# Performance work log

Hardware: AMD Instinct MI355X
Metric: run time of the kernel (lower is better)

## Reference

```python
import jax, jax.numpy as jnp
import numpy as np

D = 2048
H = 16
KV = 4
DH = D // H  # 128
REP = H // KV
ROPE_BASE = 10000.0


def _rope(x, pos):
    # x: (B, h, L, Dh), pos: (L,)
    half = x.shape[-1] // 2
    inv_freq = 1.0 / (ROPE_BASE ** (jnp.arange(0, half, dtype=jnp.float32) / half))
    ang = pos.astype(jnp.float32)[:, None] * inv_freq[None, :]          # (L, half)
    cos = jnp.concatenate([jnp.cos(ang), jnp.cos(ang)], axis=-1)        # (L, Dh)
    sin = jnp.concatenate([jnp.sin(ang), jnp.sin(ang)], axis=-1)
    x1, x2 = x[..., :half], x[..., half:]
    rot = jnp.concatenate([-x2, x1], axis=-1)
    return x * cos[None, None] + rot * sin[None, None]


def setup_inputs() -> dict:
    key = jax.random.key(0)
    ks = jax.random.split(key, 5)
    s = 1.0 / np.sqrt(D)
    return {
        "x": jax.random.normal(ks[0], (2, 2048, D), dtype=jnp.float32),
        "wq": jax.random.uniform(ks[1], (H * DH, D), jnp.float32, -s, s),
        "wk": jax.random.uniform(ks[2], (KV * DH, D), jnp.float32, -s, s),
        "wv": jax.random.uniform(ks[3], (KV * DH, D), jnp.float32, -s, s),
        "wo": jax.random.uniform(ks[4], (D, H * DH), jnp.float32, -s, s),
    }


def reference(x, wq, wk, wv, wo):
    B, T, _ = x.shape
    q = (x @ wq.T).reshape(B, T, H, DH).transpose(0, 2, 1, 3)    # (B,H,T,Dh)
    k = (x @ wk.T).reshape(B, T, KV, DH).transpose(0, 2, 1, 3)   # (B,KV,T,Dh)
    v = (x @ wv.T).reshape(B, T, KV, DH).transpose(0, 2, 1, 3)
    Tc = T  # no kv cache
    pos = jnp.arange(Tc)
    q = _rope(q, pos)
    k = _rope(k, pos)
    # GQA: repeat kv heads to match query heads
    k_full = jnp.repeat(k, REP, axis=1)                          # (B,H,Tc,Dh)
    v_full = jnp.repeat(v, REP, axis=1)
    scale = 1.0 / np.sqrt(DH)
    scores = jnp.einsum('bhtd,bhsd->bhts', q, k_full) * scale    # (B,H,T,Tc)
    row = jnp.arange(T)[:, None]
    col = jnp.arange(Tc)[None, :]
    causal = col <= row + (Tc - T)
    scores = jnp.where(causal[None, None], scores, -jnp.inf)
    attn = jax.nn.softmax(scores, axis=-1)
    out = jnp.einsum('bhts,bhsd->bhtd', attn, v_full)            # (B,H,T,Dh)
    out = out.transpose(0, 2, 1, 3).reshape(B, T, H * DH)
    return out @ wo.T
```

## Files before the change

kernel.cpp:

```cpp
#include <hip/hip_runtime.h>

typedef float f32x4 __attribute__((ext_vector_type(4)));
typedef short s16x8 __attribute__((ext_vector_type(8)));
typedef unsigned short u16;

__device__ __forceinline__ u16 f2bf(float f) {
    union { float f; unsigned u; } v; v.f = f;
    return (u16)((v.u + 0x7fffu + ((v.u >> 16) & 1u)) >> 16);
}
__device__ __forceinline__ float bf2f(u16 h) {
    union { unsigned u; float f; } v; v.u = ((unsigned)h) << 16;
    return v.f;
}
__device__ __forceinline__ float fast_exp2(float x) {
#if __has_builtin(__builtin_amdgcn_exp2f)
    return __builtin_amdgcn_exp2f(x);
#else
    return exp2f(x);
#endif
}

__device__ __forceinline__ void gload_lds16(const void* g, void* l) {
    __builtin_amdgcn_global_load_lds((__attribute__((address_space(1))) void*)g,
                                     (__attribute__((address_space(3))) void*)l, 16, 0, 0);
}

__global__ __launch_bounds__(256) void cvt_all(const float* __restrict__ x,  const float* __restrict__ wq,
                                               const float* __restrict__ wk, const float* __restrict__ wv,
                                               u16* __restrict__ xb, u16* __restrict__ wqkvb) {
    int u = blockIdx.x * 256 + threadIdx.x;
    const float* src;
    u16* dst;
    if (u < 1048576) { src = x + (size_t)u * 8; dst = xb + (size_t)u * 8; }
    else {
        int w = u - 1048576;
        dst = wqkvb + (size_t)w * 8;
        if (w < 524288)      src = wq + (size_t)w * 8;
        else if (w < 655360) src = wk + (size_t)(w - 524288) * 8;
        else                 src = wv + (size_t)(w - 655360) * 8;
    }
    const float4* p = (const float4*)src;
    float4 a = p[0], b = p[1];
    s16x8 o;
    o[0] = f2bf(a.x); o[1] = f2bf(a.y); o[2] = f2bf(a.z); o[3] = f2bf(a.w);
    o[4] = f2bf(b.x); o[5] = f2bf(b.y); o[6] = f2bf(b.z); o[7] = f2bf(b.w);
    *(s16x8*)dst = o;
}

__global__ __launch_bounds__(256) void cvt_kernel(const float* __restrict__ in,
                                                  u16* __restrict__ out, int n8) {
    int i = blockIdx.x * 256 + threadIdx.x;
    if (i >= n8) return;
    const float4* p = (const float4*)(in + (size_t)i * 8);
    float4 a = p[0], b = p[1];
    s16x8 o;
    o[0] = f2bf(a.x); o[1] = f2bf(a.y); o[2] = f2bf(a.z); o[3] = f2bf(a.w);
    o[4] = f2bf(b.x); o[5] = f2bf(b.y); o[6] = f2bf(b.z); o[7] = f2bf(b.w);
    *(s16x8*)(out + (size_t)i * 8) = o;
}

__global__ __launch_bounds__(256) void norm_comb(const float* __restrict__ Oacc,
                                                 const float* __restrict__ Lacc,
                                                 u16* __restrict__ ab) {
    int i = blockIdx.x * 256 + threadIdx.x;
    int g = i >> 15;
    int rem = i & 32767;
    int qti = rem >> 10;
    int rem2 = rem & 1023;
    int row = rem2 >> 6;
    int colblk = rem2 & 63;
    int col0 = colblk * 8;
    int head = colblk >> 4;
    size_t tile0 = (size_t)(g * 32 + qti);
    size_t tile1 = (size_t)((8 + g) * 32 + qti);
    const float* p0 = Oacc + tile0 * 8192 + row * 512 + col0;
    const float* p1 = Oacc + tile1 * 8192 + row * 512 + col0;
    float L0 = Lacc[(tile0 * 4 + head) * 16 + row];
    float L1 = Lacc[(tile1 * 4 + head) * 16 + row];
    float inv = 1.0f / (L0 + L1);
    int b = g >> 2, kv = g & 3;
    int token = (96 + qti) * 16 + row;
    u16* pd = ab + ((size_t)(b * 2048 + token) << 11) + kv * 512 + col0;
    float4 a0 = ((const float4*)p0)[0], a1 = ((const float4*)p0)[1];
    float4 b0 = ((const float4*)p1)[0], b1 = ((const float4*)p1)[1];
    s16x8 o;
    o[0] = f2bf((a0.x + b0.x) * inv); o[1] = f2bf((a0.y + b0.y) * inv);
    o[2] = f2bf((a0.z + b0.z) * inv); o[3] = f2bf((a0.w + b0.w) * inv);
    o[4] = f2bf((a1.x + b1.x) * inv); o[5] = f2bf((a1.y + b1.y) * inv);
    o[6] = f2bf((a1.z + b1.z) * inv); o[7] = f2bf((a1.w + b1.w) * inv);
    *(s16x8*)pd = o;
}

template<int OUT>
__global__ __launch_bounds__(256) void gemm128(const u16* __restrict__ A, const u16* __restrict__ B,
                                               void* __restrict__ C, void* __restrict__ Ck,
                                               void* __restrict__ Cv, int M, int N, int K) {
    __shared__ __align__(16) u16 Ald[128 * 64];
    __shared__ __align__(16) u16 Bld[128 * 64];
    const int t = threadIdx.x, wid = t >> 6, lane = t & 63;
    const int m0 = blockIdx.y * 128, n0 = blockIdx.x * 128;
    const int ml = lane & 15, quad = lane >> 4, m7 = ml & 7;
    const int wm = (wid & 1) * 64, wn = (wid >> 1) * 64;
    const int sr = lane >> 3, sc = lane & 7;

    f32x4 acc[4][4] = {};

    for (int k0 = 0; k0 < K; k0 += 64) {
        if (k0) __syncthreads();
        #pragma unroll
        for (int i = 0; i < 4; ++i) {
            int seg = wid * 4 + i;
            int r = seg * 8 + sr;
            int c = (sc ^ (r & 7)) * 8;
            gload_lds16(A + (size_t)(m0 + r) * K + k0 + c, &Ald[seg * 512]);
            gload_lds16(B + (size_t)(n0 + r) * K + k0 + c, &Bld[seg * 512]);
        }
        __syncthreads();
        #pragma unroll
        for (int kk = 0; kk < 64; kk += 32) {
            s16x8 af[4], bf[4];
            #pragma unroll
            for (int mi = 0; mi < 4; ++mi)
                af[mi] = *(const s16x8*)&Ald[(wm + mi * 16 + ml) * 64 + (((kk >> 3) + quad) ^ m7) * 8];
            #pragma unroll
            for (int ni = 0; ni < 4; ++ni)
                bf[ni] = *(const s16x8*)&Bld[(wn + ni * 16 + ml) * 64 + (((kk >> 3) + quad) ^ m7) * 8];
            #pragma unroll
            for (int mi = 0; mi < 4; ++mi)
                #pragma unroll
                for (int ni = 0; ni < 4; ++ni)
                    acc[mi][ni] = __builtin_amdgcn_mfma_f32_16x16x32_bf16(af[mi], bf[ni], acc[mi][ni], 0, 0, 0);
        }
    }
    #pragma unroll
    for (int mi = 0; mi < 4; ++mi)
        #pragma unroll
        for (int ni = 0; ni < 4; ++ni) {
            int gmb = m0 + wm + mi * 16 + quad * 4;
            int gn  = n0 + wn + ni * 16 + ml;
            if constexpr (OUT == 4) {
                if (n0 < 2048) {
                    #pragma unroll
                    for (int r = 0; r < 4; ++r)
                        ((u16*)C)[(size_t)(gmb + r) * 2048 + gn] = f2bf(acc[mi][ni][r]);
                } else if (n0 < 2560) {
                    #pragma unroll
                    for (int r = 0; r < 4; ++r)
                        ((u16*)Ck)[(size_t)(gmb + r) * 512 + (gn - 2048)] = f2bf(acc[mi][ni][r]);
                } else {
                    ushort4 v;
                    v.x = f2bf(acc[mi][ni][0]); v.y = f2bf(acc[mi][ni][1]);
                    v.z = f2bf(acc[mi][ni][2]); v.w = f2bf(acc[mi][ni][3]);
                    *(ushort4*)((u16*)Cv + (size_t)(gn - 2560) * M + gmb) = v;
                }
            } else {
                #pragma unroll
                for (int r = 0; r < 4; ++r)
                    ((float*)C)[(size_t)(gmb + r) * N + gn] = acc[mi][ni][r];
            }
        }
}

__global__ __launch_bounds__(256) void rope_kernel(u16* __restrict__ qb, u16* __restrict__ kb,
                                                   int nq, int ntot, float sq) {
    int idx = blockIdx.x * 256 + threadIdx.x;
    if (idx >= ntot) return;
    u16* base; int nheads; float scl; int id;
    if (idx < nq) { base = qb; nheads = 16; scl = sq;  id = idx; }
    else          { base = kb; nheads = 4;  scl = 1.f; id = idx - nq; }
    int i = id & 63;
    int rest = id >> 6;
    int hh = rest % nheads;
    int tok = rest / nheads;
    int tpos = tok & 2047;
    u16* row = base + (size_t)tok * nheads * 128 + hh * 128;
    float x1 = bf2f(row[i]);
    float x2 = bf2f(row[i + 64]);
    float inv = expf(-(float)i * 0.14391156731570787f);
    float ang = (float)tpos * inv;
    float s, c;
    sincosf(ang, &s, &c);
    row[i]      = f2bf((x1 * c - x2 * s) * scl);
    row[i + 64] = f2bf((x2 * c + x1 * s) * scl);
}

__global__ __launch_bounds__(256, 4) void attn_kernel(const u16* __restrict__ Q, const u16* __restrict__ Kb,
                                                      const u16* __restrict__ Vt, u16* __restrict__ O) {
    __shared__ __align__(16) u16 Klds[64 * 128];
    __shared__ __align__(16) u16 Vlds[128 * 64];
    __shared__ __align__(16) u16 Plds[4][16 * 64];
    const int t = threadIdx.x, wslot = t >> 6, lane = t & 63;
    const int kv = blockIdx.y, b = blockIdx.z;
    const int g = kv + 4 * b;
    const int bx = blockIdx.x;
    int qt;
    switch ((g >> 1) & 3) {
        case 0:  qt = bx; break;
        case 1:  qt = 127 - bx; break;
        case 2:  qt = (bx + 64) & 127; break;
        default: qt = (63 - bx) & 127; break;
    }
    const int h = kv * 4 + wslot;
    const int ml = lane & 15, quad = lane >> 4, m7 = ml & 7;
    const int t0 = qt * 16;
    const int n = (qt >> 2) + 1;

    s16x8 qf[4];
    {
        const u16* qp = Q + ((size_t)(b * 2048 + t0 + ml) * 2048 + h * 128);
        #pragma unroll
        for (int kc = 0; kc < 4; ++kc)
            qf[kc] = *(const s16x8*)(qp + kc * 32 + quad * 8);
    }

    s16x8 ones;
    #pragma unroll
    for (int j = 0; j < 8; ++j) ones[j] = (short)0x3F80;

    f32x4 Oa[8] = {};
    f32x4 L = {};

    for (int it = 0; it < n; ++it) {
        const int s0 = it * 64;
        if (it) __syncthreads();
        #pragma unroll
        for (int i = 0; i < 4; ++i) {
            int seg = wslot * 4 + i;
            int kr = seg * 4 + (lane >> 4);
            int kc = ((lane & 15) ^ (kr & 7)) * 8;
            gload_lds16(Kb + (size_t)(b * 2048 + s0 + kr) * 512 + kv * 128 + kc, &Klds[seg * 512]);
            int vr = seg * 8 + (lane >> 3);
            int vc = ((lane & 7) ^ (vr & 7)) * 8;
            gload_lds16(Vt + (size_t)(kv * 128 + vr) * 4096 + b * 2048 + s0 + vc, &Vlds[seg * 512]);
        }
        __syncthreads();

        f32x4 S[4] = {};
        #pragma unroll
        for (int kc = 0; kc < 4; ++kc)
            #pragma unroll
            for (int ti = 0; ti < 4; ++ti) {
                s16x8 kf = *(const s16x8*)&Klds[(ti * 16 + ml) * 128 + ((kc * 4 + quad) ^ m7) * 8];
                S[ti] = __builtin_amdgcn_mfma_f32_16x16x32_bf16(qf[kc], kf, S[ti], 0, 0, 0);
            }

        {
            u16* pl = &Plds[wslot][0];
            const bool diag = (it == n - 1);
            #pragma unroll
            for (int r = 0; r < 4; ++r) {
                int qr = t0 + quad * 4 + r;
                int row = quad * 4 + r;
                #pragma unroll
                for (int ti = 0; ti < 4; ++ti) {
                    float e = fast_exp2(S[ti][r]);
                    if (diag && (s0 + ti * 16 + ml > qr)) e = 0.f;
                    union { float f; unsigned u; } cv; cv.f = e;
                    pl[row * 64 + (((ti * 2 + (ml >> 3)) ^ (row & 7)) * 8) + (ml & 7)] = (u16)(cv.u >> 16);
                }
            }
        }
        asm volatile("s_waitcnt lgkmcnt(0)" ::: "memory");
        s16x8 pf[2];
        pf[0] = *(const s16x8*)&Plds[wslot][ml * 64 + ((quad)     ^ m7) * 8];
        pf[1] = *(const s16x8*)&Plds[wslot][ml * 64 + ((4 + quad) ^ m7) * 8];
        asm volatile("s_waitcnt lgkmcnt(0)" ::: "memory");

        #pragma unroll
        for (int c = 0; c < 2; ++c) {
            #pragma unroll
            for (int nt = 0; nt < 8; ++nt) {
                s16x8 vf = *(const s16x8*)&Vlds[(nt * 16 + ml) * 64 + ((c * 4 + quad) ^ m7) * 8];
                Oa[nt] = __builtin_amdgcn_mfma_f32_16x16x32_bf16(pf[c], vf, Oa[nt], 0, 0, 0);
            }
            L = __builtin_amdgcn_mfma_f32_16x16x32_bf16(pf[c], ones, L, 0, 0, 0);
        }
    }

    #pragma unroll
    for (int nt = 0; nt < 8; ++nt)
        #pragma unroll
        for (int r = 0; r < 4; ++r) {
            int col = h * 128 + nt * 16 + ml;
            O[(size_t)(b * 2048 + t0 + quad * 4 + r) * 2048 + col] = f2bf(Oa[nt][r] / L[r]);
        }
}

__global__ __launch_bounds__(256, 4) void attn_sched(const u16* __restrict__ Q, const u16* __restrict__ Kb,
                                                     const u16* __restrict__ Vt, u16* __restrict__ O,
                                                     float* __restrict__ Oacc, float* __restrict__ Lacc) {
    __shared__ __align__(16) u16 Klds[64 * 128];
    __shared__ __align__(16) u16 Vlds[128 * 64];
    __shared__ __align__(16) u16 Plds[4][16 * 64];
    const int t = threadIdx.x, wslot = t >> 6, lane = t & 63;
    const int bid = blockIdx.x;
    const int idx = bid >> 3, g = bid & 7;
    const int kv = g & 3, b = g >> 2;

    int qt, it0, it1, nfull, hsel = 0;
    bool partial;
    if (idx < 32) {
        qt = 95 - idx; nfull = (qt >> 2) + 1; it0 = 0; it1 = nfull; partial = false;
    } else if (idx < 96) {
        int p = (idx - 32) >> 1; hsel = (idx - 32) & 1;
        qt = 127 - p; nfull = (qt >> 2) + 1;
        int nh = nfull >> 1;
        it0 = hsel ? nh : 0;
        it1 = hsel ? nfull : nh;
        partial = true;
    } else {
        qt = 159 - idx; nfull = (qt >> 2) + 1; it0 = 0; it1 = nfull; partial = false;
    }

    const int h = kv * 4 + wslot;
    const int ml = lane & 15, quad = lane >> 4, m7 = ml & 7;
    const int t0 = qt * 16;

    s16x8 qf[4];
    {
        const u16* qp = Q + ((size_t)(b * 2048 + t0 + ml) * 2048 + h * 128);
        #pragma unroll
        for (int kc = 0; kc < 4; ++kc)
            qf[kc] = *(const s16x8*)(qp + kc * 32 + quad * 8);
    }

    s16x8 ones;
    #pragma unroll
    for (int j = 0; j < 8; ++j) ones[j] = (short)0x3F80;

    f32x4 Oa[8] = {};
    f32x4 L = {};

    for (int it = it0; it < it1; ++it) {
        const int s0 = it * 64;
        if (it != it0) __syncthreads();
        #pragma unroll
        for (int i = 0; i < 4; ++i) {
            int seg = wslot * 4 + i;
            int kr = seg * 4 + (lane >> 4);
            int kc = ((lane & 15) ^ (kr & 7)) * 8;
            gload_lds16(Kb + (size_t)(b * 2048 + s0 + kr) * 512 + kv * 128 + kc, &Klds[seg * 512]);
            int vr = seg * 8 + (lane >> 3);
            int vc = ((lane & 7) ^ (vr & 7)) * 8;
            gload_lds16(Vt + (size_t)(kv * 128 + vr) * 4096 + b * 2048 + s0 + vc, &Vlds[seg * 512]);
        }
        __syncthreads();

        f32x4 S[4] = {};
        #pragma unroll
        for (int kc = 0; kc < 4; ++kc)
            #pragma unroll
            for (int ti = 0; ti < 4; ++ti) {
                s16x8 kf = *(const s16x8*)&Klds[(ti * 16 + ml) * 128 + ((kc * 4 + quad) ^ m7) * 8];
                S[ti] = __builtin_amdgcn_mfma_f32_16x16x32_bf16(qf[kc], kf, S[ti], 0, 0, 0);
            }

        {
            u16* pl = &Plds[wslot][0];
            const bool diag = (it == nfull - 1);
            #pragma unroll
            for (int r = 0; r < 4; ++r) {
                int qr = t0 + quad * 4 + r;
                int row = quad * 4 + r;
                #pragma unroll
                for (int ti = 0; ti < 4; ++ti) {
                    float e = fast_exp2(S[ti][r]);
                    if (diag && (s0 + ti * 16 + ml > qr)) e = 0.f;
                    union { float f; unsigned u; } cv; cv.f = e;
                    pl[row * 64 + (((ti * 2 + (ml >> 3)) ^ (row & 7)) * 8) + (ml & 7)] = (u16)(cv.u >> 16);
                }
            }
        }
        asm volatile("s_waitcnt lgkmcnt(0)" ::: "memory");
        s16x8 pf[2];
        pf[0] = *(const s16x8*)&Plds[wslot][ml * 64 + ((quad)     ^ m7) * 8];
        pf[1] = *(const s16x8*)&Plds[wslot][ml * 64 + ((4 + quad) ^ m7) * 8];
        asm volatile("s_waitcnt lgkmcnt(0)" ::: "memory");

        #pragma unroll
        for (int c = 0; c < 2; ++c) {
            #pragma unroll
            for (int nt = 0; nt < 8; ++nt) {
                s16x8 vf = *(const s16x8*)&Vlds[(nt * 16 + ml) * 64 + ((c * 4 + quad) ^ m7) * 8];
                Oa[nt] = __builtin_amdgcn_mfma_f32_16x16x32_bf16(pf[c], vf, Oa[nt], 0, 0, 0);
            }
            L = __builtin_amdgcn_mfma_f32_16x16x32_bf16(pf[c], ones, L, 0, 0, 0);
        }
    }

    if (!partial) {
        #pragma unroll
        for (int nt = 0; nt < 8; ++nt)
            #pragma unroll
            for (int r = 0; r < 4; ++r) {
                int col = h * 128 + nt * 16 + ml;
                O[(size_t)(b * 2048 + t0 + quad * 4 + r) * 2048 + col] = f2bf(Oa[nt][r] / L[r]);
            }
    } else {
        const int qti = qt - 96;
        float* Ob = Oacc + (size_t)((hsel * 8 + g) * 32 + qti) * 8192;
        #pragma unroll
        for (int nt = 0; nt < 8; ++nt)
            #pragma unroll
            for (int r = 0; r < 4; ++r)
                Ob[(quad * 4 + r) * 512 + wslot * 128 + nt * 16 + ml] = Oa[nt][r];
        if (ml == 0) {
            float* Lb = Lacc + ((size_t)((hsel * 8 + g) * 32 + qti) * 4 + wslot) * 16;
            #pragma unroll
            for (int r = 0; r < 4; ++r)
                Lb[quad * 4 + r] = L[r];
        }
    }
}

extern "C" void kernel_launch(void* const* d_in, const int* in_sizes, int n_in,
                              void* d_out, int out_size, void* d_ws, size_t ws_size,
                              hipStream_t stream) {
    const float* x  = (const float*)d_in[0];
    const float* wq = (const float*)d_in[1];
    const float* wk = (const float*)d_in[2];
    const float* wv = (const float*)d_in[3];
    const float* wo = (const float*)d_in[4];
    float* out = (float*)d_out;
    char* ws = (char*)d_ws;

    const size_t MB = 1024 * 1024;
    u16* xb    = (u16*)(ws);
    u16* qb    = (u16*)(ws + 16 * MB);
    u16* kb    = (u16*)(ws + 32 * MB);
    u16* vtb   = (u16*)(ws + 36 * MB);
    u16* wqkvb = (u16*)(ws + 40 * MB);
    u16* ab    = xb;
    u16* wob   = wqkvb;

    const bool split = ws_size >= 70 * MB;

    cvt_all<<<7168, 256, 0, stream>>>(x, wq, wk, wv, xb, wqkvb);

    gemm128<4><<<dim3(24, 32), 256, 0, stream>>>(xb, wqkvb, qb, kb, vtb, 4096, 3072, 2048);

    cvt_kernel<<<2048, 256, 0, stream>>>(wo, wob, 524288);

    rope_kernel<<<20480, 256, 0, stream>>>(qb, kb, 4194304, 5242880, 0.12751743f);

    if (split) {
        float* Oacc = (float*)(ws + 52 * MB);
        float* Lacc = (float*)(ws + 68 * MB);
        attn_sched<<<1280, 256, 0, stream>>>(qb, kb, vtb, ab, Oacc, Lacc);
        norm_comb<<<1024, 256, 0, stream>>>(Oacc, Lacc, ab);
    } else {
        attn_kernel<<<dim3(128, 4, 2), 256, 0, stream>>>(qb, kb, vtb, ab);
    }

    gemm128<1><<<dim3(16, 32), 256, 0, stream>>>(ab, wob, out, nullptr, nullptr, 4096, 2048, 2048);
}
```

Measured before the change: 323.8 us.

## Process paired 16-row query tiles per block to reuse K/V LDS loads

The attention kernel now handles two 16-row query tiles (32 query rows) per block. Each K/V tile staged in LDS is reused for twice as many MFMA operations, and the grid shrinks from 1280 to 768 blocks with a reworked causal split schedule. Partial accumulators are written into the output buffer as scratch, which lowers the workspace threshold needed to enable the split path. The cost is doubled accumulator registers, with launch bounds lowered to 3 blocks per CU, so occupancy may drop.

```diff
diff --git a/kernel.cpp b/kernel.cpp
--- a/kernel.cpp
+++ b/kernel.cpp
@@ -59,28 +59,27 @@
     *(s16x8*)(out + (size_t)i * 8) = o;
 }
 
-__global__ __launch_bounds__(256) void norm_comb(const float* __restrict__ Oacc,
-                                                 const float* __restrict__ Lacc,
+__global__ __launch_bounds__(256) void norm_comb(const float* __restrict__ Opart,
+                                                 const float* __restrict__ Lpart,
                                                  u16* __restrict__ ab) {
     int i = blockIdx.x * 256 + threadIdx.x;
-    int g = i >> 15;
-    int rem = i & 32767;
-    int qti = rem >> 10;
-    int rem2 = rem & 1023;
-    int row = rem2 >> 6;
-    int colblk = rem2 & 63;
-    int col0 = colblk * 8;
-    int head = colblk >> 4;
-    size_t tile0 = (size_t)(g * 32 + qti);
-    size_t tile1 = (size_t)((8 + g) * 32 + qti);
-    const float* p0 = Oacc + tile0 * 8192 + row * 512 + col0;
-    const float* p1 = Oacc + tile1 * 8192 + row * 512 + col0;
-    float L0 = Lacc[(tile0 * 4 + head) * 16 + row];
-    float L1 = Lacc[(tile1 * 4 + head) * 16 + row];
+    int c0 = (i & 63) * 8;
+    int r2 = i >> 6;
+    int row32 = r2 & 31;
+    int r3 = r2 >> 5;
+    int qsi = r3 & 31;
+    int g = r3 >> 5;
+    int head = c0 >> 7;
+    size_t pi0 = (size_t)(g * 32 + qsi);
+    size_t pi1 = (size_t)((8 + g) * 32 + qsi);
+    const float* p0 = Opart + pi0 * 16384 + row32 * 512 + c0;
+    const float* p1 = Opart + pi1 * 16384 + row32 * 512 + c0;
+    float L0 = Lpart[pi0 * 128 + row32 * 4 + head];
+    float L1 = Lpart[pi1 * 128 + row32 * 4 + head];
     float inv = 1.0f / (L0 + L1);
     int b = g >> 2, kv = g & 3;
-    int token = (96 + qti) * 16 + row;
-    u16* pd = ab + ((size_t)(b * 2048 + token) << 11) + kv * 512 + col0;
+    int token = (32 + qsi) * 32 + row32;
+    u16* pd = ab + ((size_t)(b * 2048 + token) << 11) + kv * 512 + c0;
     float4 a0 = ((const float4*)p0)[0], a1 = ((const float4*)p0)[1];
     float4 b0 = ((const float4*)p1)[0], b1 = ((const float4*)p1)[1];
     s16x8 o;
@@ -286,50 +285,53 @@
         }
 }
 
-__global__ __launch_bounds__(256, 4) void attn_sched(const u16* __restrict__ Q, const u16* __restrict__ Kb,
-                                                     const u16* __restrict__ Vt, u16* __restrict__ O,
-                                                     float* __restrict__ Oacc, float* __restrict__ Lacc) {
+__global__ __launch_bounds__(256, 3) void attn_pair(const u16* __restrict__ Q, const u16* __restrict__ Kb,
+                                                    const u16* __restrict__ Vt, u16* __restrict__ O,
+                                                    float* __restrict__ Opart, float* __restrict__ Lpart) {
     __shared__ __align__(16) u16 Klds[64 * 128];
     __shared__ __align__(16) u16 Vlds[128 * 64];
-    __shared__ __align__(16) u16 Plds[4][16 * 64];
+    __shared__ __align__(16) u16 Plds[4][2][16 * 64];
     const int t = threadIdx.x, wslot = t >> 6, lane = t & 63;
     const int bid = blockIdx.x;
-    const int idx = bid >> 3, g = bid & 7;
+    const int g = bid & 7, idx = bid >> 3;
     const int kv = g & 3, b = g >> 2;
 
-    int qt, it0, it1, nfull, hsel = 0;
+    int qs, it0, it1, n, hsel = 0;
     bool partial;
-    if (idx < 32) {
-        qt = 95 - idx; nfull = (qt >> 2) + 1; it0 = 0; it1 = nfull; partial = false;
-    } else if (idx < 96) {
-        int p = (idx - 32) >> 1; hsel = (idx - 32) & 1;
-        qt = 127 - p; nfull = (qt >> 2) + 1;
-        int nh = nfull >> 1;
+    if (idx < 64) {
+        int p = idx >> 1; hsel = idx & 1;
+        qs = 63 - p; n = (qs >> 1) + 1;
+        int nh = n >> 1;
         it0 = hsel ? nh : 0;
-        it1 = hsel ? nfull : nh;
+        it1 = hsel ? n : nh;
         partial = true;
     } else {
-        qt = 159 - idx; nfull = (qt >> 2) + 1; it0 = 0; it1 = nfull; partial = false;
+        qs = 95 - idx; n = (qs >> 1) + 1;
+        it0 = 0; it1 = n;
+        partial = false;
     }
 
     const int h = kv * 4 + wslot;
     const int ml = lane & 15, quad = lane >> 4, m7 = ml & 7;
-    const int t0 = qt * 16;
-
-    s16x8 qf[4];
+    const int t0a = qs * 32, t0b = qs * 32 + 16;
+
+    s16x8 qfA[4], qfB[4];
     {
-        const u16* qp = Q + ((size_t)(b * 2048 + t0 + ml) * 2048 + h * 128);
-        #pragma unroll
-        for (int kc = 0; kc < 4; ++kc)
-            qf[kc] = *(const s16x8*)(qp + kc * 32 + quad * 8);
+        const u16* qpA = Q + ((size_t)(b * 2048 + t0a + ml) * 2048 + h * 128);
+        const u16* qpB = Q + ((size_t)(b * 2048 + t0b + ml) * 2048 + h * 128);
+        #pragma unroll
+        for (int kc = 0; kc < 4; ++kc) {
+            qfA[kc] = *(const s16x8*)(qpA + kc * 32 + quad * 8);
+            qfB[kc] = *(const s16x8*)(qpB + kc * 32 + quad * 8);
+        }
     }
 
     s16x8 ones;
     #pragma unroll
     for (int j = 0; j < 8; ++j) ones[j] = (short)0x3F80;
 
-    f32x4 Oa[8] = {};
-    f32x4 L = {};
+    f32x4 OA[8] = {}, OB[8] = {};
+    f32x4 LA = {}, LB = {};
 
     for (int it = it0; it < it1; ++it) {
         const int s0 = it * 64;
@@ -346,18 +348,19 @@
         }
         __syncthreads();
 
-        f32x4 S[4] = {};
+        f32x4 Sa[4] = {}, Sb[4] = {};
         #pragma unroll
         for (int kc = 0; kc < 4; ++kc)
             #pragma unroll
             for (int ti = 0; ti < 4; ++ti) {
                 s16x8 kf = *(const s16x8*)&Klds[(ti * 16 + ml) * 128 + ((kc * 4 + quad) ^ m7) * 8];
-                S[ti] = __builtin_amdgcn_mfma_f32_16x16x32_bf16(qf[kc], kf, S[ti], 0, 0, 0);
-            }
-
-        {
-            u16* pl = &Plds[wslot][0];
-            const bool diag = (it == nfull - 1);
+                Sa[ti] = __builtin_amdgcn_mfma_f32_16x16x32_bf16(qfA[kc], kf, Sa[ti], 0, 0, 0);
+                Sb[ti] = __builtin_amdgcn_mfma_f32_16x16x32_bf16(qfB[kc], kf, Sb[ti], 0, 0, 0);
+            }
+
+        const bool diag = (it == n - 1);
+        auto do_soft = [&](f32x4* S, int t0, int pslot) {
+            u16* pl = &Plds[wslot][pslot][0];
             #pragma unroll
             for (int r = 0; r < 4; ++r) {
                 int qr = t0 + quad * 4 + r;
@@ -370,11 +373,15 @@
                     pl[row * 64 + (((ti * 2 + (ml >> 3)) ^ (row & 7)) * 8) + (ml & 7)] = (u16)(cv.u >> 16);
                 }
             }
-        }
+        };
+        do_soft(Sa, t0a, 0);
+        do_soft(Sb, t0b, 1);
         asm volatile("s_waitcnt lgkmcnt(0)" ::: "memory");
-        s16x8 pf[2];
-        pf[0] = *(const s16x8*)&Plds[wslot][ml * 64 + ((quad)     ^ m7) * 8];
-        pf[1] = *(const s16x8*)&Plds[wslot][ml * 64 + ((4 + quad) ^ m7) * 8];
+        s16x8 pfA[2], pfB[2];
+        pfA[0] = *(const s16x8*)&Plds[wslot][0][ml * 64 + ((quad)     ^ m7) * 8];
+        pfA[1] = *(const s16x8*)&Plds[wslot][0][ml * 64 + ((4 + quad) ^ m7) * 8];
+        pfB[0] = *(const s16x8*)&Plds[wslot][1][ml * 64 + ((quad)     ^ m7) * 8];
+        pfB[1] = *(const s16x8*)&Plds[wslot][1][ml * 64 + ((4 + quad) ^ m7) * 8];
         asm volatile("s_waitcnt lgkmcnt(0)" ::: "memory");
 
         #pragma unroll
@@ -382,9 +389,11 @@
             #pragma unroll
             for (int nt = 0; nt < 8; ++nt) {
                 s16x8 vf = *(const s16x8*)&Vlds[(nt * 16 + ml) * 64 + ((c * 4 + quad) ^ m7) * 8];
-                Oa[nt] = __builtin_amdgcn_mfma_f32_16x16x32_bf16(pf[c], vf, Oa[nt], 0, 0, 0);
-            }
-            L = __builtin_amdgcn_mfma_f32_16x16x32_bf16(pf[c], ones, L, 0, 0, 0);
+                OA[nt] = __builtin_amdgcn_mfma_f32_16x16x32_bf16(pfA[c], vf, OA[nt], 0, 0, 0);
+                OB[nt] = __builtin_amdgcn_mfma_f32_16x16x32_bf16(pfB[c], vf, OB[nt], 0, 0, 0);
+            }
+            LA = __builtin_amdgcn_mfma_f32_16x16x32_bf16(pfA[c], ones, LA, 0, 0, 0);
+            LB = __builtin_amdgcn_mfma_f32_16x16x32_bf16(pfB[c], ones, LB, 0, 0, 0);
         }
     }
 
@@ -394,21 +403,27 @@
             #pragma unroll
             for (int r = 0; r < 4; ++r) {
                 int col = h * 128 + nt * 16 + ml;
-                O[(size_t)(b * 2048 + t0 + quad * 4 + r) * 2048 + col] = f2bf(Oa[nt][r] / L[r]);
+                O[(size_t)(b * 2048 + t0a + quad * 4 + r) * 2048 + col] = f2bf(OA[nt][r] / LA[r]);
+                O[(size_t)(b * 2048 + t0b + quad * 4 + r) * 2048 + col] = f2bf(OB[nt][r] / LB[r]);
             }
     } else {
-        const int qti = qt - 96;
-        float* Ob = Oacc + (size_t)((hsel * 8 + g) * 32 + qti) * 8192;
+        const size_t pi = (size_t)((hsel * 8 + g) * 32 + (qs - 32));
+        float* Ob = Opart + pi * 16384;
+        float* Lb = Lpart + pi * 128;
         #pragma unroll
         for (int nt = 0; nt < 8; ++nt)
             #pragma unroll
-            for (int r = 0; r < 4; ++r)
-                Ob[(quad * 4 + r) * 512 + wslot * 128 + nt * 16 + ml] = Oa[nt][r];
+            for (int r = 0; r < 4; ++r) {
+                int c = wslot * 128 + nt * 16 + ml;
+                Ob[(quad * 4 + r) * 512 + c]        = OA[nt][r];
+                Ob[(16 + quad * 4 + r) * 512 + c]   = OB[nt][r];
+            }
         if (ml == 0) {
-            float* Lb = Lacc + ((size_t)((hsel * 8 + g) * 32 + qti) * 4 + wslot) * 16;
-            #pragma unroll
-            for (int r = 0; r < 4; ++r)
-                Lb[quad * 4 + r] = L[r];
+            #pragma unroll
+            for (int r = 0; r < 4; ++r) {
+                Lb[(quad * 4 + r) * 4 + wslot]      = LA[r];
+                Lb[(16 + quad * 4 + r) * 4 + wslot] = LB[r];
+            }
         }
     }
 }
@@ -433,7 +448,7 @@
     u16* ab    = xb;
     u16* wob   = wqkvb;
 
-    const bool split = ws_size >= 70 * MB;
+    const bool split = ws_size >= 53 * MB;
 
     cvt_all<<<7168, 256, 0, stream>>>(x, wq, wk, wv, xb, wqkvb);
 
@@ -444,10 +459,10 @@
     rope_kernel<<<20480, 256, 0, stream>>>(qb, kb, 4194304, 5242880, 0.12751743f);
 
     if (split) {
-        float* Oacc = (float*)(ws + 52 * MB);
-        float* Lacc = (float*)(ws + 68 * MB);
-        attn_sched<<<1280, 256, 0, stream>>>(qb, kb, vtb, ab, Oacc, Lacc);
-        norm_comb<<<1024, 256, 0, stream>>>(Oacc, Lacc, ab);
+        float* Opart = out;
+        float* Lpart = (float*)(ws + 52 * MB);
+        attn_pair<<<768, 256, 0, stream>>>(qb, kb, vtb, ab, Opart, Lpart);
+        norm_comb<<<2048, 256, 0, stream>>>(Opart, Lpart, ab);
     } else {
         attn_kernel<<<dim3(128, 4, 2), 256, 0, stream>>>(qb, kb, vtb, ab);
     }
```

Result: slower. 351.9 us (+8.7%).

## Split attention KV loop for all upper-half query tiles, stage partials in output buffer

Applied to the files above, without the earlier changes.

Extends the split-KV scheme so that all query tiles from 64 to 127 are processed by two half-blocks, where before only tiles 96 to 127 were. Grid size grows from 1280 to 1536 blocks, and norm_comb grows to match. This is meant to balance the causal workload across CUs. The float partial-output buffer now lives in the final output tensor, which the out-projection GEMM later overwrites. That lowers the workspace requirement so the split path is taken more often, at the cost of more partial-sum traffic and more combine work.

```diff
diff --git a/kernel.cpp b/kernel.cpp
--- a/kernel.cpp
+++ b/kernel.cpp
@@ -59,28 +59,27 @@
     *(s16x8*)(out + (size_t)i * 8) = o;
 }
 
-__global__ __launch_bounds__(256) void norm_comb(const float* __restrict__ Oacc,
-                                                 const float* __restrict__ Lacc,
+__global__ __launch_bounds__(256) void norm_comb(const float* __restrict__ Opart,
+                                                 const float* __restrict__ Lpart,
                                                  u16* __restrict__ ab) {
     int i = blockIdx.x * 256 + threadIdx.x;
-    int g = i >> 15;
-    int rem = i & 32767;
-    int qti = rem >> 10;
-    int rem2 = rem & 1023;
-    int row = rem2 >> 6;
-    int colblk = rem2 & 63;
-    int col0 = colblk * 8;
-    int head = colblk >> 4;
-    size_t tile0 = (size_t)(g * 32 + qti);
-    size_t tile1 = (size_t)((8 + g) * 32 + qti);
-    const float* p0 = Oacc + tile0 * 8192 + row * 512 + col0;
-    const float* p1 = Oacc + tile1 * 8192 + row * 512 + col0;
-    float L0 = Lacc[(tile0 * 4 + head) * 16 + row];
-    float L1 = Lacc[(tile1 * 4 + head) * 16 + row];
+    int c0 = (i & 63) * 8;
+    int r = i >> 6;
+    int row = r & 15;
+    int r2 = r >> 4;
+    int qti = r2 & 63;
+    int g = r2 >> 6;
+    int head = c0 >> 7;
+    size_t pi0 = (size_t)(g * 64 + qti);
+    size_t pi1 = (size_t)((8 + g) * 64 + qti);
+    const float* p0 = Opart + pi0 * 8192 + row * 512 + c0;
+    const float* p1 = Opart + pi1 * 8192 + row * 512 + c0;
+    float L0 = Lpart[pi0 * 64 + row * 4 + head];
+    float L1 = Lpart[pi1 * 64 + row * 4 + head];
     float inv = 1.0f / (L0 + L1);
     int b = g >> 2, kv = g & 3;
-    int token = (96 + qti) * 16 + row;
-    u16* pd = ab + ((size_t)(b * 2048 + token) << 11) + kv * 512 + col0;
+    int token = (64 + qti) * 16 + row;
+    u16* pd = ab + ((size_t)(b * 2048 + token) << 11) + kv * 512 + c0;
     float4 a0 = ((const float4*)p0)[0], a1 = ((const float4*)p0)[1];
     float4 b0 = ((const float4*)p1)[0], b1 = ((const float4*)p1)[1];
     s16x8 o;
@@ -288,7 +287,7 @@
 
 __global__ __launch_bounds__(256, 4) void attn_sched(const u16* __restrict__ Q, const u16* __restrict__ Kb,
                                                      const u16* __restrict__ Vt, u16* __restrict__ O,
-                                                     float* __restrict__ Oacc, float* __restrict__ Lacc) {
+                                                     float* __restrict__ Opart, float* __restrict__ Lpart) {
     __shared__ __align__(16) u16 Klds[64 * 128];
     __shared__ __align__(16) u16 Vlds[128 * 64];
     __shared__ __align__(16) u16 Plds[4][16 * 64];
@@ -297,19 +296,17 @@
     const int idx = bid >> 3, g = bid & 7;
     const int kv = g & 3, b = g >> 2;
 
-    int qt, it0, it1, nfull, hsel = 0;
+    int qt, it0, it1, n, hsel = 0;
     bool partial;
-    if (idx < 32) {
-        qt = 95 - idx; nfull = (qt >> 2) + 1; it0 = 0; it1 = nfull; partial = false;
-    } else if (idx < 96) {
-        int p = (idx - 32) >> 1; hsel = (idx - 32) & 1;
-        qt = 127 - p; nfull = (qt >> 2) + 1;
-        int nh = nfull >> 1;
+    if (idx < 64) {
+        qt = 63 - idx; n = (qt >> 2) + 1; it0 = 0; it1 = n; partial = false;
+    } else {
+        int p = (idx - 64) >> 1; hsel = (idx - 64) & 1;
+        qt = 127 - p; n = (qt >> 2) + 1;
+        int nh = n >> 1;
         it0 = hsel ? nh : 0;
-        it1 = hsel ? nfull : nh;
+        it1 = hsel ? n : nh;
         partial = true;
-    } else {
-        qt = 159 - idx; nfull = (qt >> 2) + 1; it0 = 0; it1 = nfull; partial = false;
     }
 
     const int h = kv * 4 + wslot;
@@ -357,7 +354,7 @@
 
         {
             u16* pl = &Plds[wslot][0];
-            const bool diag = (it == nfull - 1);
+            const bool diag = (it == n - 1);
             #pragma unroll
             for (int r = 0; r < 4; ++r) {
                 int qr = t0 + quad * 4 + r;
@@ -397,18 +394,19 @@
                 O[(size_t)(b * 2048 + t0 + quad * 4 + r) * 2048 + col] = f2bf(Oa[nt][r] / L[r]);
             }
     } else {
-        const int qti = qt - 96;
-        float* Ob = Oacc + (size_t)((hsel * 8 + g) * 32 + qti) * 8192;
+        const int qti = qt - 64;
+        const size_t pi = (size_t)((hsel * 8 + g) * 64 + qti);
+        float* Ob = Opart + pi * 8192;
         #pragma unroll
         for (int nt = 0; nt < 8; ++nt)
             #pragma unroll
             for (int r = 0; r < 4; ++r)
                 Ob[(quad * 4 + r) * 512 + wslot * 128 + nt * 16 + ml] = Oa[nt][r];
         if (ml == 0) {
-            float* Lb = Lacc + ((size_t)((hsel * 8 + g) * 32 + qti) * 4 + wslot) * 16;
+            float* Lb = Lpart + pi * 64;
             #pragma unroll
             for (int r = 0; r < 4; ++r)
-                Lb[quad * 4 + r] = L[r];
+                Lb[(quad * 4 + r) * 4 + wslot] = L[r];
         }
     }
 }
@@ -433,7 +431,7 @@
     u16* ab    = xb;
     u16* wob   = wqkvb;
 
-    const bool split = ws_size >= 70 * MB;
+    const bool split = ws_size >= 53 * MB;
 
     cvt_all<<<7168, 256, 0, stream>>>(x, wq, wk, wv, xb, wqkvb);
 
@@ -444,10 +442,10 @@
     rope_kernel<<<20480, 256, 0, stream>>>(qb, kb, 4194304, 5242880, 0.12751743f);
 
     if (split) {
-        float* Oacc = (float*)(ws + 52 * MB);
-        float* Lacc = (float*)(ws + 68 * MB);
-        attn_sched<<<1280, 256, 0, stream>>>(qb, kb, vtb, ab, Oacc, Lacc);
-        norm_comb<<<1024, 256, 0, stream>>>(Oacc, Lacc, ab);
+        float* Opart = out;
+        float* Lpart = (float*)(ws + 52 * MB);
+        attn_sched<<<1536, 256, 0, stream>>>(qb, kb, vtb, ab, Opart, Lpart);
+        norm_comb<<<2048, 256, 0, stream>>>(Opart, Lpart, ab);
     } else {
         attn_kernel<<<dim3(128, 4, 2), 256, 0, stream>>>(qb, kb, vtb, ab);
     }
```

Measured after the change: 316.0 us. 2.4% less time.
